# Optimization experiments

Measured on AMD Instinct MI355X. Metric: run time of the kernel, lower is better.

The kernel has to match this reference:

```python
import jax, jax.numpy as jnp
import numpy as np
from jax import lax

FACTOR = 2
GAIN = 1.0
RESAMPLE = (1.0, 3.0, 3.0, 1.0)


def _setup_fir():
    k = np.asarray(RESAMPLE, dtype=np.float32)
    k = np.outer(k, k)
    k /= k.sum()
    return k * (GAIN * FACTOR ** 2)  # 4x4, scaled by factor^2 for upsampling


def setup_inputs() -> dict:
    key = jax.random.key(0)
    k1, k2, k3 = jax.random.split(key, 3)
    x = jax.random.normal(k1, (16, 256, 64, 64), jnp.float32)
    weight = jax.random.normal(k2, (256, 256, 3, 3), jnp.float32) * 0.05
    bias = jax.random.normal(k3, (256,), jnp.float32) * 0.05
    return {"x": x, "weight": weight, "bias": bias}


def _upsample_conv_2d(x, w):
    # Equivalent to torch: conv_transpose2d(x, flip(w).transpose(0,1), stride=FACTOR)
    # The pre-flip cancels conv_transpose's kernel flip, so this is an
    # input-dilated cross-correlation with the original OIHW weight.
    outC, inC, kh, kw = w.shape
    y = lax.conv_general_dilated(
        x, w, window_strides=(1, 1),
        padding=[(kh - 1, kh - 1), (kw - 1, kw - 1)],
        lhs_dilation=(FACTOR, FACTOR),
        dimension_numbers=('NCHW', 'OIHW', 'NCHW'))  # (N, outC, (H-1)*f+kh, (W-1)*f+kw)

    # upfirdn2d(y, fir, up=1, down=1, pad=((p+1)//2 + factor-1, p//2 + 1))
    fir = jnp.asarray(_setup_fir())
    fh, fw = fir.shape
    p = fh - FACTOR - (kw - 1)  # = 0 for k=3, factor=2, 4-tap FIR
    pad0 = (p + 1) // 2 + FACTOR - 1  # = 1
    pad1 = p // 2 + 1                  # = 1
    # upfirdn2d_native correlates with the flipped FIR, depthwise per channel
    dw = jnp.broadcast_to(fir[::-1, ::-1], (outC, 1, fh, fw))
    out = lax.conv_general_dilated(
        y, dw, window_strides=(1, 1),
        padding=[(pad0, pad1), (pad0, pad1)],
        feature_group_count=outC,
        dimension_numbers=('NCHW', 'OIHW', 'NCHW'))  # (N, outC, H*f, W*f)
    return out


def reference(x, weight, bias):
    out = _upsample_conv_2d(x, weight)
    return out + bias.reshape(1, -1, 1, 1)
```

## Files before the change

kernel.cpp:

```cpp
#include <hip/hip_runtime.h>
#include <hip/hip_bf16.h>

using bf16 = __hip_bfloat16;
typedef __bf16 bf16x8 __attribute__((ext_vector_type(8)));
typedef float f32x4 __attribute__((ext_vector_type(4)));
typedef short short8 __attribute__((ext_vector_type(8)));
typedef _Float16 h2 __attribute__((ext_vector_type(2)));

#define AS1(p) ((const __attribute__((address_space(1))) void*)(p))
#define AS3(p) ((__attribute__((address_space(3))) void*)(p))

#define YSTRIDE 4368

__global__ void prep_wt_k(const float* __restrict__ w, bf16* __restrict__ wt) {
  const int o = blockIdx.x, i = threadIdx.x;
  const float* wp = w + (size_t)(o * 256 + i) * 9;
#pragma unroll
  for (int p = 0; p < 9; ++p)
    wt[(size_t)p * 65536 + o * 256 + i] = __float2bfloat16(wp[p]);
}

__global__ void zring_k(bf16* __restrict__ xpad) {
  const int bid = blockIdx.x;
  const int n = bid / 33, cg = bid - n * 33;
  const int t = threadIdx.x;
  const int cell = cg * 8 + (t >> 5);
  if (cell >= 260) return;
  int row, col;
  if (cell < 66) { row = 0; col = cell; }
  else if (cell < 132) { row = 65; col = cell - 66; }
  else if (cell < 196) { row = cell - 131; col = 0; }
  else { row = cell - 195; col = 65; }
  const int ch = (t & 31) * 8;
  short8 z = {0, 0, 0, 0, 0, 0, 0, 0};
  *(short8*)(xpad + (((size_t)n * 66 + row) * 66 + col) * 256 + ch) = z;
}

__global__ void xpose_k(const float* __restrict__ x, bf16* __restrict__ xpad) {
  const int b = blockIdx.x;
  const int icb = b & 3, iy = (b >> 2) & 63, n = b >> 8;
  __shared__ bf16 lds[64][72];
  const int t = threadIdx.x;
  const int c = t & 63, ixg = t >> 6;
  const float* src = x + (((size_t)(n * 256 + icb * 64 + c) * 64 + iy) * 64);
#pragma unroll
  for (int rep = 0; rep < 4; ++rep) {
    const int ix0 = ixg * 16 + rep * 4;
    float4 v = *reinterpret_cast<const float4*>(src + ix0);
    lds[ix0 + 0][c] = __float2bfloat16(v.x);
    lds[ix0 + 1][c] = __float2bfloat16(v.y);
    lds[ix0 + 2][c] = __float2bfloat16(v.z);
    lds[ix0 + 3][c] = __float2bfloat16(v.w);
  }
  __syncthreads();
  const int ix = t >> 2, cseg = (t & 3) * 16;
  bf16* dst = xpad + (((size_t)(n * 66 + iy + 1) * 66 + ix + 1) * 256 + icb * 64 + cseg);
  *reinterpret_cast<short8*>(dst) = *reinterpret_cast<const short8*>(&lds[ix][cseg]);
  *reinterpret_cast<short8*>(dst + 8) = *reinterpret_cast<const short8*>(&lds[ix][cseg + 8]);
}

__device__ __forceinline__ int xcdswz(int b, int n) {
  const int q = n >> 3, r = n & 7;
  const int xcd = b & 7, idx = b >> 3;
  return (xcd < r ? xcd * (q + 1) : r * (q + 1) + (xcd - r) * q) + idx;
}

template <int PLANE>
__device__ __forceinline__ void passA_body(int bid, const bf16* __restrict__ xpad,
                                           const bf16* __restrict__ wt,
                                           _Float16* __restrict__ yy, int nimg,
                                           bf16* ldsW, bf16* ldsX) {
  constexpr int M = (PLANE == 0) ? 4225 : (PLANE == 3) ? 4096 : 4160;
  constexpr int T = (M + 255) >> 8;
  constexpr int NT = (PLANE == 0) ? 4 : (PLANE == 3) ? 1 : 2;
  constexpr int NK = NT * 4;
  constexpr int AOFF = (PLANE >= 2) ? 1 : 0;
  constexpr int BOFF = (PLANE & 1) ? 1 : 0;
  constexpr int TAPI_all[4][4] = {{0, 2, 6, 8}, {1, 7, 0, 0}, {3, 5, 0, 0}, {4, 0, 0, 0}};
  constexpr int TDY_all[4][4] = {{0, 0, 1, 1}, {0, 1, 0, 0}, {0, 0, 0, 0}, {0, 0, 0, 0}};
  constexpr int TDX_all[4][4] = {{0, 1, 0, 1}, {0, 0, 0, 0}, {0, 1, 0, 0}, {0, 0, 0, 0}};

  const int t = threadIdx.x;
  const int tile = bid % T;
  const int nl = bid / T;
  const int m0 = tile * 256;
  const bf16* xn = xpad + (size_t)nl * (66 * 66 * 256);
  _Float16* yn = yy + ((size_t)(PLANE * nimg + nl) * 256) * YSTRIDE;

  const int w = t >> 6, lane = t & 63;
  const int wr = w >> 1, wc = w & 1;
  const int lr = lane & 15, lg = lane >> 4;

  auto dec = [](int m, int& a, int& b) {
    if (PLANE == 0 || PLANE == 2) { a = m / 65; b = m - a * 65; }
    else { a = m >> 6; b = m & 63; }
  };

  int wOffB[4], xOffB[4];
#pragma unroll
  for (int r = 0; r < 4; ++r) {
    const int idx = r * 512 + t;
    const int row = idx >> 3;
    const int swz = ((idx & 7) * 16) ^ ((row & 7) << 4);
    wOffB[r] = (row * 256) * 2 + swz;
    int m = m0 + row;
    if (m >= M) m = 0;
    int a, b;
    dec(m, a, b);
    xOffB[r] = (((a + AOFF) * 66 + (b + BOFF)) * 256) * 2 + swz;
  }

  auto stage = [&](int ks, int buf) {
    const int ti = ks >> 2, icb = ks & 3;
    const int xtoff = ((TDY_all[PLANE][ti] * 66 + TDX_all[PLANE][ti]) * 256 + icb * 64) * 2;
    const int wtoff = (TAPI_all[PLANE][ti] * 65536 + icb * 64) * 2;
    bf16* lw = ldsW + (size_t)buf * (256 * 64);
    bf16* lx = ldsX + (size_t)buf * (256 * 64);
#pragma unroll
    for (int r = 0; r < 4; ++r) {
      __builtin_amdgcn_global_load_lds(AS1((const char*)wt + wOffB[r] + wtoff),
                                       AS3(lw + (size_t)(r * 512 + (t & 448)) * 8), 16, 0, 0);
      __builtin_amdgcn_global_load_lds(AS1((const char*)xn + xOffB[r] + xtoff),
                                       AS3(lx + (size_t)(r * 512 + (t & 448)) * 8), 16, 0, 0);
    }
  };

  f32x4 acc[4][8];
#pragma unroll
  for (int i = 0; i < 4; ++i)
#pragma unroll
    for (int j = 0; j < 8; ++j) acc[i][j] = (f32x4){0.f, 0.f, 0.f, 0.f};

  stage(0, 0);
  __syncthreads();

  for (int ks = 0; ks < NK; ++ks) {
    const int cur = ks & 1;
    if (ks + 1 < NK) stage(ks + 1, cur ^ 1);
    const bf16* lw = ldsW + (size_t)cur * (256 * 64);
    const bf16* lx = ldsX + (size_t)cur * (256 * 64);
#pragma unroll
    for (int kk = 0; kk < 2; ++kk) {
      bf16x8 af[4], bfr[8];
#pragma unroll
      for (int i = 0; i < 4; ++i) {
        const int row = wr * 64 + i * 16 + lr;
        const int off = row * 128 + ((kk * 64 + lg * 16) ^ ((row & 7) << 4));
        af[i] = *(const bf16x8*)((const char*)lw + off);
      }
#pragma unroll
      for (int j = 0; j < 8; ++j) {
        const int row = wc * 128 + j * 16 + lr;
        const int off = row * 128 + ((kk * 64 + lg * 16) ^ ((row & 7) << 4));
        bfr[j] = *(const bf16x8*)((const char*)lx + off);
      }
#pragma unroll
      for (int i = 0; i < 4; ++i)
#pragma unroll
        for (int j = 0; j < 8; ++j)
          acc[i][j] = __builtin_amdgcn_mfma_f32_16x16x32_bf16(af[i], bfr[j], acc[i][j], 0, 0, 0);
    }
    __syncthreads();
  }

#pragma unroll
  for (int i = 0; i < 4; ++i) {
    const int ocb = wr * 64 + i * 16 + lg * 4;
#pragma unroll
    for (int j = 0; j < 8; ++j) {
      const int m = m0 + wc * 128 + j * 16 + lr;
      if (m < M) {
        int a, b;
        dec(m, a, b);
        const size_t sp = (size_t)(a + 1) * 66 + (b + 1);
#pragma unroll
        for (int reg = 0; reg < 4; ++reg)
          yn[(size_t)(ocb + reg) * YSTRIDE + sp] = (_Float16)acc[i][j][reg];
      }
    }
  }
}

__global__ __launch_bounds__(512) void passA_all(const bf16* __restrict__ xpad,
                                                 const bf16* __restrict__ wt,
                                                 _Float16* __restrict__ yy, int nimg) {
  __shared__ __attribute__((aligned(16))) bf16 ldsW[2][256 * 64];
  __shared__ __attribute__((aligned(16))) bf16 ldsX[2][256 * 64];
  int bid = blockIdx.x;
  const int S0 = nimg * 17, S1 = nimg * 17, S2 = nimg * 17;
  if (bid < S0) { passA_body<0>(xcdswz(bid, S0), xpad, wt, yy, nimg, &ldsW[0][0], &ldsX[0][0]); return; }
  bid -= S0;
  if (bid < S1) { passA_body<1>(xcdswz(bid, S1), xpad, wt, yy, nimg, &ldsW[0][0], &ldsX[0][0]); return; }
  bid -= S1;
  if (bid < S2) { passA_body<2>(xcdswz(bid, S2), xpad, wt, yy, nimg, &ldsW[0][0], &ldsX[0][0]); return; }
  bid -= S2;
  passA_body<3>(xcdswz(bid, nimg * 16), xpad, wt, yy, nimg, &ldsW[0][0], &ldsX[0][0]);
}

#define BSTRIDE 2248

__global__ void passB_k(const _Float16* __restrict__ yy, const float* __restrict__ bias,
                        float* __restrict__ out, int nimg, int n0) {
  __shared__ _Float16 ldsY[4][BSTRIDE];
  const int b = blockIdx.x;
  const int h = b & 1, c = (b >> 1) & 255, nl = b >> 9;
  const int R0 = h * 32;
  const int t = threadIdx.x;
  const size_t PS = (size_t)nimg * 256 * YSTRIDE;
  const _Float16* base = yy + ((size_t)nl * 256 + c) * YSTRIDE;

  for (int idx = t; idx < 4 * 281; idx += 256) {
    const int pl = idx / 281, off = idx - pl * 281;
    *(float4*)(&ldsY[pl][off * 8]) =
        *(const float4*)((const char*)(base + (size_t)pl * PS) + R0 * 132 + (size_t)off * 16);
  }
  __syncthreads();
  const int brel = h ? 33 : 0;
  for (int idx = t; idx < 268; idx += 256) {
    if (idx < 68) {
      const int r = idx >> 1, col = (idx & 1) * 65;
      ldsY[1][r * 66 + col] = (_Float16)0.f;
    } else if (idx < 134) {
      ldsY[2][brel * 66 + (idx - 68)] = (_Float16)0.f;
    } else if (idx < 200) {
      ldsY[3][brel * 66 + (idx - 134)] = (_Float16)0.f;
    } else {
      const int k = idx - 200;
      const int r = k >> 1, col = (k & 1) * 65;
      ldsY[3][r * 66 + col] = (_Float16)0.f;
    }
  }
  __syncthreads();

  const int q = t & 31, g = t >> 5;
  const float bv = bias[c];
  float* ob = out + ((size_t)(n0 + nl) * 256 + c) * 16384;
  const int r0 = g * 4;

  float eeA[4], eeB[4], oeA[4], oeB[4], oeC[4];
  float eoA[4], eoB[4], ooA[4], ooB[4], ooC[4];

#define LD4(dst, pl, row)                                          \
  { const h2 u0 = *(const h2*)(&ldsY[pl][(row) * 66 + 2 * q]);     \
    const h2 u1 = *(const h2*)(&ldsY[pl][(row) * 66 + 2 * q + 2]); \
    dst[0] = (float)u0[0]; dst[1] = (float)u0[1];                  \
    dst[2] = (float)u1[0]; dst[3] = (float)u1[1]; }

  LD4(eeA, 0, r0 + 1); LD4(eeB, 0, r0 + 2);
  LD4(oeA, 2, r0);     LD4(oeB, 2, r0 + 1); LD4(oeC, 2, r0 + 2);
  LD4(eoA, 1, r0 + 1); LD4(eoB, 1, r0 + 2);
  LD4(ooA, 3, r0);     LD4(ooB, 3, r0 + 1); LD4(ooC, 3, r0 + 2);

#pragma unroll
  for (int oi = 0; oi < 4; ++oi) {
    const int o = R0 + r0 + oi;
    float rceq[2][3], rcoq[2][4];
#pragma unroll
    for (int k = 0; k < 3; ++k) {
      const int vi = k + 1;
      rceq[0][k] = 0.75f * eeA[vi] + 0.25f * eeB[vi] + 0.25f * oeA[vi] + 0.75f * oeB[vi];
      rceq[1][k] = 0.25f * eeA[vi] + 0.75f * eeB[vi] + 0.75f * oeB[vi] + 0.25f * oeC[vi];
    }
#pragma unroll
    for (int k = 0; k < 4; ++k) {
      rcoq[0][k] = 0.75f * eoA[k] + 0.25f * eoB[k] + 0.25f * ooA[k] + 0.75f * ooB[k];
      rcoq[1][k] = 0.25f * eoA[k] + 0.75f * eoB[k] + 0.75f * ooB[k] + 0.25f * ooC[k];
    }
#pragma unroll
    for (int py = 0; py < 2; ++py) {
      float4 st;
      st.x = 0.75f * rceq[py][0] + 0.25f * rceq[py][1] + 0.25f * rcoq[py][0] +
             0.75f * rcoq[py][1] + bv;
      st.y = 0.25f * rceq[py][0] + 0.75f * rceq[py][1] + 0.75f * rcoq[py][1] +
             0.25f * rcoq[py][2] + bv;
      st.z = 0.75f * rceq[py][1] + 0.25f * rceq[py][2] + 0.25f * rcoq[py][1] +
             0.75f * rcoq[py][2] + bv;
      st.w = 0.25f * rceq[py][1] + 0.75f * rceq[py][2] + 0.75f * rcoq[py][2] +
             0.25f * rcoq[py][3] + bv;
      *(float4*)(ob + ((size_t)(2 * o + py)) * 128 + 4 * q) = st;
    }
    if (oi < 3) {
#pragma unroll
      for (int k = 0; k < 4; ++k) {
        eeA[k] = eeB[k]; oeA[k] = oeB[k]; oeB[k] = oeC[k];
        eoA[k] = eoB[k]; ooA[k] = ooB[k]; ooB[k] = ooC[k];
      }
      LD4(eeB, 0, r0 + oi + 3);
      LD4(oeC, 2, r0 + oi + 3);
      LD4(eoB, 1, r0 + oi + 3);
      LD4(ooC, 3, r0 + oi + 3);
    }
  }
#undef LD4
}

extern "C" void kernel_launch(void* const* d_in, const int* in_sizes, int n_in,
                              void* d_out, int out_size, void* d_ws, size_t ws_size,
                              hipStream_t stream) {
  const float* x = (const float*)d_in[0];
  const float* wgt = (const float*)d_in[1];
  const float* bias = (const float*)d_in[2];
  float* out = (float*)d_out;

  const size_t XPL = (size_t)66 * 66 * 256;
  const size_t YPN = (size_t)4 * 256 * YSTRIDE;
  const size_t WT_BYTES = (size_t)9 * 256 * 256 * 2;
  int c = 0;
  const int cands[5] = {16, 8, 4, 2, 1};
  for (int ci = 0; ci < 5; ++ci)
    if (WT_BYTES + (size_t)cands[ci] * (XPL + YPN) * 2 <= ws_size) { c = cands[ci]; break; }
  if (c == 0) return;

  bf16* wt = (bf16*)d_ws;
  bf16* xpad = (bf16*)((char*)d_ws + WT_BYTES);
  _Float16* yy = (_Float16*)((char*)d_ws + WT_BYTES + (size_t)c * XPL * 2);

  prep_wt_k<<<256, 256, 0, stream>>>(wgt, wt);

  for (int k = 0; k < 16 / c; ++k) {
    zring_k<<<c * 33, 256, 0, stream>>>(xpad);
    xpose_k<<<c * 256, 256, 0, stream>>>(x + (size_t)k * c * 1048576, xpad);
    passA_all<<<c * 67, 512, 0, stream>>>(xpad, wt, yy, c);
    passB_k<<<c * 512, 256, 0, stream>>>(yy, bias, out, c, k * c);
  }
}
```

Baseline: 239.1 us.

## Deepen passA pipeline to 4 LDS stages with half-size K steps and vmcnt waits

```diff
diff --git a/kernel.cpp b/kernel.cpp
--- a/kernel.cpp
+++ b/kernel.cpp
@@ -65,6 +65,8 @@
   return (xcd < r ? xcd * (q + 1) : r * (q + 1) + (xcd - r) * q) + idx;
 }
 
+#define WAITV(N) asm volatile("s_waitcnt vmcnt(" N ")" ::: "memory")
+
 template <int PLANE>
 __device__ __forceinline__ void passA_body(int bid, const bf16* __restrict__ xpad,
                                            const bf16* __restrict__ wt,
@@ -73,7 +75,7 @@
   constexpr int M = (PLANE == 0) ? 4225 : (PLANE == 3) ? 4096 : 4160;
   constexpr int T = (M + 255) >> 8;
   constexpr int NT = (PLANE == 0) ? 4 : (PLANE == 3) ? 1 : 2;
-  constexpr int NK = NT * 4;
+  constexpr int NS = NT * 8;
   constexpr int AOFF = (PLANE >= 2) ? 1 : 0;
   constexpr int BOFF = (PLANE & 1) ? 1 : 0;
   constexpr int TAPI_all[4][4] = {{0, 2, 6, 8}, {1, 7, 0, 0}, {3, 5, 0, 0}, {4, 0, 0, 0}};
@@ -96,28 +98,28 @@
     else { a = m >> 6; b = m & 63; }
   };
 
-  int wOffB[4], xOffB[4];
-#pragma unroll
-  for (int r = 0; r < 4; ++r) {
+  int wOffB[2], xOffB[2];
+#pragma unroll
+  for (int r = 0; r < 2; ++r) {
     const int idx = r * 512 + t;
-    const int row = idx >> 3;
-    const int swz = ((idx & 7) * 16) ^ ((row & 7) << 4);
-    wOffB[r] = (row * 256) * 2 + swz;
+    const int row = idx >> 2;
+    const int swz16 = ((idx & 3) ^ ((row >> 1) & 3)) * 16;
+    wOffB[r] = row * 512 + swz16;
     int m = m0 + row;
     if (m >= M) m = 0;
     int a, b;
     dec(m, a, b);
-    xOffB[r] = (((a + AOFF) * 66 + (b + BOFF)) * 256) * 2 + swz;
-  }
-
-  auto stage = [&](int ks, int buf) {
-    const int ti = ks >> 2, icb = ks & 3;
-    const int xtoff = ((TDY_all[PLANE][ti] * 66 + TDX_all[PLANE][ti]) * 256 + icb * 64) * 2;
-    const int wtoff = (TAPI_all[PLANE][ti] * 65536 + icb * 64) * 2;
-    bf16* lw = ldsW + (size_t)buf * (256 * 64);
-    bf16* lx = ldsX + (size_t)buf * (256 * 64);
-#pragma unroll
-    for (int r = 0; r < 4; ++r) {
+    xOffB[r] = ((a + AOFF) * 66 + (b + BOFF)) * 512 + swz16;
+  }
+
+  auto stage = [&](int ks2, int buf) {
+    const int ti = ks2 >> 3, icb = ks2 & 7;
+    const int xtoff = (TDY_all[PLANE][ti] * 66 + TDX_all[PLANE][ti]) * 512 + icb * 64;
+    const int wtoff = TAPI_all[PLANE][ti] * 131072 + icb * 64;
+    bf16* lw = ldsW + (size_t)buf * 8192;
+    bf16* lx = ldsX + (size_t)buf * 8192;
+#pragma unroll
+    for (int r = 0; r < 2; ++r) {
       __builtin_amdgcn_global_load_lds(AS1((const char*)wt + wOffB[r] + wtoff),
                                        AS3(lw + (size_t)(r * 512 + (t & 448)) * 8), 16, 0, 0);
       __builtin_amdgcn_global_load_lds(AS1((const char*)xn + xOffB[r] + xtoff),
@@ -125,6 +127,18 @@
     }
   };
 
+  int aOff[4], bOff[8];
+#pragma unroll
+  for (int i = 0; i < 4; ++i) {
+    const int row = wr * 64 + i * 16 + lr;
+    aOff[i] = row * 64 + ((lg ^ ((row >> 1) & 3)) * 16);
+  }
+#pragma unroll
+  for (int j = 0; j < 8; ++j) {
+    const int row = wc * 128 + j * 16 + lr;
+    bOff[j] = row * 64 + ((lg ^ ((row >> 1) & 3)) * 16);
+  }
+
   f32x4 acc[4][8];
 #pragma unroll
   for (int i = 0; i < 4; ++i)
@@ -132,35 +146,32 @@
     for (int j = 0; j < 8; ++j) acc[i][j] = (f32x4){0.f, 0.f, 0.f, 0.f};
 
   stage(0, 0);
-  __syncthreads();
-
-  for (int ks = 0; ks < NK; ++ks) {
-    const int cur = ks & 1;
-    if (ks + 1 < NK) stage(ks + 1, cur ^ 1);
-    const bf16* lw = ldsW + (size_t)cur * (256 * 64);
-    const bf16* lx = ldsX + (size_t)cur * (256 * 64);
-#pragma unroll
-    for (int kk = 0; kk < 2; ++kk) {
-      bf16x8 af[4], bfr[8];
-#pragma unroll
-      for (int i = 0; i < 4; ++i) {
-        const int row = wr * 64 + i * 16 + lr;
-        const int off = row * 128 + ((kk * 64 + lg * 16) ^ ((row & 7) << 4));
-        af[i] = *(const bf16x8*)((const char*)lw + off);
-      }
-#pragma unroll
-      for (int j = 0; j < 8; ++j) {
-        const int row = wc * 128 + j * 16 + lr;
-        const int off = row * 128 + ((kk * 64 + lg * 16) ^ ((row & 7) << 4));
-        bfr[j] = *(const bf16x8*)((const char*)lx + off);
-      }
-#pragma unroll
-      for (int i = 0; i < 4; ++i)
-#pragma unroll
-        for (int j = 0; j < 8; ++j)
-          acc[i][j] = __builtin_amdgcn_mfma_f32_16x16x32_bf16(af[i], bfr[j], acc[i][j], 0, 0, 0);
-    }
-    __syncthreads();
+  stage(1, 1);
+  stage(2, 2);
+
+  for (int i = 0; i < NS; ++i) {
+    if (i < NS - 2) WAITV("8");
+    else if (i == NS - 2) WAITV("4");
+    else WAITV("0");
+    __builtin_amdgcn_s_barrier();
+    __builtin_amdgcn_sched_barrier(0);
+    if (i + 3 < NS) stage(i + 3, (i + 3) & 3);
+
+    const char* lw = (const char*)(ldsW + (size_t)(i & 3) * 8192);
+    const char* lx = (const char*)(ldsX + (size_t)(i & 3) * 8192);
+    bf16x8 af[4], bfr[8];
+#pragma unroll
+    for (int i4 = 0; i4 < 4; ++i4) af[i4] = *(const bf16x8*)(lw + aOff[i4]);
+#pragma unroll
+    for (int j = 0; j < 8; ++j) bfr[j] = *(const bf16x8*)(lx + bOff[j]);
+
+    __builtin_amdgcn_s_setprio(1);
+#pragma unroll
+    for (int i4 = 0; i4 < 4; ++i4)
+#pragma unroll
+      for (int j = 0; j < 8; ++j)
+        acc[i4][j] = __builtin_amdgcn_mfma_f32_16x16x32_bf16(af[i4], bfr[j], acc[i4][j], 0, 0, 0);
+    __builtin_amdgcn_s_setprio(0);
   }
 
 #pragma unroll
@@ -184,8 +195,8 @@
 __global__ __launch_bounds__(512) void passA_all(const bf16* __restrict__ xpad,
                                                  const bf16* __restrict__ wt,
                                                  _Float16* __restrict__ yy, int nimg) {
-  __shared__ __attribute__((aligned(16))) bf16 ldsW[2][256 * 64];
-  __shared__ __attribute__((aligned(16))) bf16 ldsX[2][256 * 64];
+  __shared__ __attribute__((aligned(16))) bf16 ldsW[4][8192];
+  __shared__ __attribute__((aligned(16))) bf16 ldsX[4][8192];
   int bid = blockIdx.x;
   const int S0 = nimg * 17, S1 = nimg * 17, S2 = nimg * 17;
   if (bid < S0) { passA_body<0>(xcdswz(bid, S0), xpad, wt, yy, nimg, &ldsW[0][0], &ldsX[0][0]); return; }
```

Result: slower. 253.8 us (+6.1%).

## Reuse one staged input tile across all taps via row-shifted LDS reads

Applied to the files above, without the earlier changes.

```diff
diff --git a/kernel.cpp b/kernel.cpp
--- a/kernel.cpp
+++ b/kernel.cpp
@@ -73,12 +73,16 @@
   constexpr int M = (PLANE == 0) ? 4225 : (PLANE == 3) ? 4096 : 4160;
   constexpr int T = (M + 255) >> 8;
   constexpr int NT = (PLANE == 0) ? 4 : (PLANE == 3) ? 1 : 2;
-  constexpr int NK = NT * 4;
+  constexpr int NSTEP = NT * 4;
   constexpr int AOFF = (PLANE >= 2) ? 1 : 0;
   constexpr int BOFF = (PLANE & 1) ? 1 : 0;
+  constexpr int DW = (PLANE == 0 || PLANE == 2) ? 65 : 64;
   constexpr int TAPI_all[4][4] = {{0, 2, 6, 8}, {1, 7, 0, 0}, {3, 5, 0, 0}, {4, 0, 0, 0}};
   constexpr int TDY_all[4][4] = {{0, 0, 1, 1}, {0, 1, 0, 0}, {0, 0, 0, 0}, {0, 0, 0, 0}};
   constexpr int TDX_all[4][4] = {{0, 1, 0, 1}, {0, 0, 0, 0}, {0, 1, 0, 0}, {0, 0, 0, 0}};
+  constexpr int MAXS = TDY_all[PLANE][NT - 1] * DW + TDX_all[PLANE][NT - 1];
+  constexpr int UR = 256 + MAXS;
+  constexpr int XBUF = 328 * 64;
 
   const int t = threadIdx.x;
   const int tile = bid % T;
@@ -96,49 +100,73 @@
     else { a = m >> 6; b = m & 63; }
   };
 
-  int wOffB[4], xOffB[4];
+  int wOffB[4];
 #pragma unroll
   for (int r = 0; r < 4; ++r) {
     const int idx = r * 512 + t;
     const int row = idx >> 3;
-    const int swz = ((idx & 7) * 16) ^ ((row & 7) << 4);
-    wOffB[r] = (row * 256) * 2 + swz;
-    int m = m0 + row;
-    if (m >= M) m = 0;
-    int a, b;
-    dec(m, a, b);
-    xOffB[r] = (((a + AOFF) * 66 + (b + BOFF)) * 256) * 2 + swz;
-  }
-
-  auto stage = [&](int ks, int buf) {
-    const int ti = ks >> 2, icb = ks & 3;
-    const int xtoff = ((TDY_all[PLANE][ti] * 66 + TDX_all[PLANE][ti]) * 256 + icb * 64) * 2;
-    const int wtoff = (TAPI_all[PLANE][ti] * 65536 + icb * 64) * 2;
+    wOffB[r] = (row * 256) * 2 + (((idx & 7) * 16) ^ ((row & 7) << 4));
+  }
+
+  int xOffU[6];
+  const int nxc = (UR * 8 - t + 511) >> 9;
+#pragma unroll
+  for (int k = 0; k < 6; ++k) {
+    const int cidx = k * 512 + t;
+    if (cidx < UR * 8) {
+      const int row = cidx >> 3;
+      const int swz = ((cidx & 7) * 16) ^ ((row & 7) << 4);
+      const int ms = m0 + row;
+      if (ms < M) {
+        int a, b;
+        dec(ms, a, b);
+        xOffU[k] = (((a + AOFF) * 66 + (b + BOFF)) * 256) * 2 + swz;
+      } else {
+        xOffU[k] = (65 * 66 * 256) * 2 + swz;
+      }
+    }
+  }
+
+  auto stage_w = [&](int step, int buf) {
+    const int tap = step % NT, icb = step / NT;
+    const int wtoff = (TAPI_all[PLANE][tap] * 65536 + icb * 64) * 2;
     bf16* lw = ldsW + (size_t)buf * (256 * 64);
-    bf16* lx = ldsX + (size_t)buf * (256 * 64);
-#pragma unroll
-    for (int r = 0; r < 4; ++r) {
+#pragma unroll
+    for (int r = 0; r < 4; ++r)
       __builtin_amdgcn_global_load_lds(AS1((const char*)wt + wOffB[r] + wtoff),
                                        AS3(lw + (size_t)(r * 512 + (t & 448)) * 8), 16, 0, 0);
-      __builtin_amdgcn_global_load_lds(AS1((const char*)xn + xOffB[r] + xtoff),
-                                       AS3(lx + (size_t)(r * 512 + (t & 448)) * 8), 16, 0, 0);
-    }
   };
 
+  auto stage_x = [&](int icb, int buf) {
+    const int xtoffB = icb * 128;
+    bf16* lx = ldsX + (size_t)buf * XBUF;
+    for (int k = 0; k < nxc; ++k) {
+      const int cidx = k * 512 + t;
+      __builtin_amdgcn_global_load_lds(AS1((const char*)xn + xOffU[k] + xtoffB),
+                                       AS3(lx + (size_t)(cidx & ~63) * 8), 16, 0, 0);
+    }
+  };
+
   f32x4 acc[4][8];
 #pragma unroll
   for (int i = 0; i < 4; ++i)
 #pragma unroll
     for (int j = 0; j < 8; ++j) acc[i][j] = (f32x4){0.f, 0.f, 0.f, 0.f};
 
-  stage(0, 0);
+  stage_w(0, 0);
+  stage_x(0, 0);
   __syncthreads();
 
-  for (int ks = 0; ks < NK; ++ks) {
-    const int cur = ks & 1;
-    if (ks + 1 < NK) stage(ks + 1, cur ^ 1);
-    const bf16* lw = ldsW + (size_t)cur * (256 * 64);
-    const bf16* lx = ldsX + (size_t)cur * (256 * 64);
+  for (int step = 0; step < NSTEP; ++step) {
+    const int icb = step / NT, tap = step - icb * NT;
+    const int next = step + 1;
+    if (next < NSTEP) {
+      stage_w(next, next & 1);
+      if (next - (next / NT) * NT == 0) stage_x(next / NT, (next / NT) & 1);
+    }
+    const int sOff = TDY_all[PLANE][tap] * DW + TDX_all[PLANE][tap];
+    const bf16* lw = ldsW + (size_t)(step & 1) * (256 * 64);
+    const bf16* lx = ldsX + (size_t)(icb & 1) * XBUF;
 #pragma unroll
     for (int kk = 0; kk < 2; ++kk) {
       bf16x8 af[4], bfr[8];
@@ -150,7 +178,7 @@
       }
 #pragma unroll
       for (int j = 0; j < 8; ++j) {
-        const int row = wc * 128 + j * 16 + lr;
+        const int row = wc * 128 + j * 16 + lr + sOff;
         const int off = row * 128 + ((kk * 64 + lg * 16) ^ ((row & 7) << 4));
         bfr[j] = *(const bf16x8*)((const char*)lx + off);
       }
@@ -185,7 +213,7 @@
                                                  const bf16* __restrict__ wt,
                                                  _Float16* __restrict__ yy, int nimg) {
   __shared__ __attribute__((aligned(16))) bf16 ldsW[2][256 * 64];
-  __shared__ __attribute__((aligned(16))) bf16 ldsX[2][256 * 64];
+  __shared__ __attribute__((aligned(16))) bf16 ldsX[2][328 * 64];
   int bid = blockIdx.x;
   const int S0 = nimg * 17, S1 = nimg * 17, S2 = nimg * 17;
   if (bid < S0) { passA_body<0>(xcdswz(bid, S0), xpad, wt, yy, nimg, &ldsW[0][0], &ldsX[0][0]); return; }
```

After: 236.5 us. Within noise of the previous version (-1.1%).
